# Optimization experiments

Measured on AMD Instinct MI355X. Metric: run time of the kernel, lower is better.

The kernel has to match this reference:

```python
import jax, jax.numpy as jnp
import numpy as np
import math

B, S, D = 4, 512, 2048
NH, DEG = 8, 4            # chebyshev heads / degree
HD = D // NH              # 256
AH = 16                   # attention heads
AHD = D // AH             # 128
W = 512                   # local attention window
BASE_LR = 0.005

def rmsnorm(x, w, eps=1e-6):
    return x * jax.lax.rsqrt(jnp.mean(x * x, axis=-1, keepdims=True) + eps) * w

def cheby_rkv(xn, coeffs, momentum, gate, ema):
    # Chebyshev spectral read + EMA/TTT coefficient update (apply_cheby_rkv_v10)
    Bb, Ss, Dd = xn.shape
    u = xn.reshape(Bb, Ss, NH, HD)
    z = jnp.tanh(u.mean(-1))                       # (B,S,NH) in [-1,1]
    Ts = [jnp.ones_like(z), z]
    for _ in range(DEG - 2):
        Ts.append(2.0 * z * Ts[-1] - Ts[-2])       # Chebyshev recurrence
    T = jnp.stack(Ts[:DEG], axis=-1)               # (B,S,NH,DEG)
    out = jnp.einsum('bshk,bhkd->bshd', T, coeffs).reshape(Bb, Ss, Dd)
    grad = jnp.einsum('bshk,bshd->bhkd', T, u) / Ss
    mom = ema * momentum + (1.0 - ema) * grad
    coeffs_new = coeffs + BASE_LR * gate[:, :, None, None] * mom
    return out, coeffs_new, mom

def local_attention(q, k, v):
    # q,k,v: (B,H,S,hd); causal attention within a sliding window of W
    Bb, H, Ss, hd = q.shape
    nc = Ss // W
    q = q.reshape(Bb, H, nc, W, hd)
    k = k.reshape(Bb, H, nc, W, hd)
    v = v.reshape(Bb, H, nc, W, hd)
    kprev = jnp.concatenate([jnp.zeros_like(k[:, :, :1]), k[:, :, :-1]], axis=2)
    vprev = jnp.concatenate([jnp.zeros_like(v[:, :, :1]), v[:, :, :-1]], axis=2)
    kk = jnp.concatenate([kprev, k], axis=3)       # (B,H,nc,2W,hd)
    vv = jnp.concatenate([vprev, v], axis=3)
    qi = jnp.arange(W)
    kj = jnp.arange(2 * W)
    causal = (kj[None, :] - W) <= qi[:, None]      # (W,2W)
    chunk_ok = (jnp.arange(nc)[:, None, None] > 0) | (kj[None, None, :] >= W)
    mask = causal[None] & chunk_ok                 # (nc,W,2W)
    scores = jnp.einsum('bhnqd,bhnkd->bhnqk', q, kk) / math.sqrt(hd)
    scores = jnp.where(mask[None, None], scores, -1e9)
    attn = jax.nn.softmax(scores, axis=-1)
    o = jnp.einsum('bhnqk,bhnkd->bhnqd', attn, vv)
    return o.reshape(Bb, H, Ss, hd)

def _forward(x, w_in, wg1, bg1, wg2, bg2, wc1, bc1, wc2, bc2,
             wq, wk, wv, wo, w_nc, w_ns, w_fgv, w_np, w_out):
    Bb, Ss, Dd = x.shape
    xn = rmsnorm(x, w_in)
    x_mean = xn.mean(axis=1)                       # (B,D)
    # coeff init (cheby_state is None): MLP + spectral 1/(k+1) scaling
    h = jax.nn.silu(x_mean @ wc1 + bc1)
    coeff_raw = h @ wc2 + bc2
    kidx = jnp.arange(DEG, dtype=jnp.float32)
    spectral_scale = (0.1 / (kidx + 1.0)).reshape(1, 1, DEG, 1)
    coeffs = coeff_raw.reshape(Bb, NH, DEG, HD) * spectral_scale
    momentum = jnp.zeros_like(coeffs)
    # complexity gate (GatedComplexityPredictor)
    g = jax.nn.silu(x_mean @ wg1 + bg1)
    gate_global = jax.nn.sigmoid(g @ wg2 + bg2)    # (B,1)
    # EMA momentum schedule: total_tokens_seen = S after this call
    progress = min(Ss / 1e8, 1.0)
    ema = 0.7 + 0.5 * (0.9 - 0.7) * (1.0 + math.cos(progress * math.pi))
    cheby_out, coeffs, momentum = cheby_rkv(xn, coeffs, momentum, gate_global, ema)
    # SLR: windowed local attention, keys/values conditioned on cheby output
    kv_src = xn + cheby_out
    q = (xn @ wq).reshape(Bb, Ss, AH, AHD).transpose(0, 2, 1, 3)
    k = (kv_src @ wk).reshape(Bb, Ss, AH, AHD).transpose(0, 2, 1, 3)
    v = (kv_src @ wv).reshape(Bb, Ss, AH, AHD).transpose(0, 2, 1, 3)
    slr = local_attention(q, k, v).transpose(0, 2, 1, 3).reshape(Bb, Ss, Dd) @ wo
    # gated SwiGLU-style fusion of the two paths
    h1 = rmsnorm(cheby_out, w_nc)
    h2 = rmsnorm(slr, w_ns)
    gv = jnp.concatenate([h1, h2], axis=-1) @ w_fgv
    gate, value = gv[..., :Dd], gv[..., Dd:]
    fused = rmsnorm(jax.nn.silu(gate) * value, w_np)
    return x + fused @ w_out

def setup_inputs() -> dict:
    key = jax.random.key(0)
    ks = jax.random.split(key, 12)
    s = 0.02
    return {
        'x': jax.random.normal(ks[0], (B, S, D), jnp.float32),
        'w_in': jnp.ones((D,), jnp.float32),
        'wg1': jax.random.normal(ks[1], (D, D // 4), jnp.float32) * s,
        'bg1': jnp.zeros((D // 4,), jnp.float32),
        'wg2': jax.random.normal(ks[2], (D // 4, 1), jnp.float32) * s,
        'bg2': jnp.zeros((1,), jnp.float32),
        'wc1': jax.random.normal(ks[3], (D, D // 4), jnp.float32) * s,
        'bc1': jnp.zeros((D // 4,), jnp.float32),
        'wc2': jax.random.normal(ks[4], (D // 4, NH * DEG * HD), jnp.float32) * s,
        'bc2': jnp.zeros((NH * DEG * HD,), jnp.float32),
        'wq': jax.random.normal(ks[5], (D, D), jnp.float32) * s,
        'wk': jax.random.normal(ks[6], (D, D), jnp.float32) * s,
        'wv': jax.random.normal(ks[7], (D, D), jnp.float32) * s,
        'wo': jax.random.normal(ks[8], (D, D), jnp.float32) * s,
        'w_nc': jnp.ones((D,), jnp.float32),
        'w_ns': jnp.ones((D,), jnp.float32),
        'w_fgv': jax.random.normal(ks[9], (2 * D, 2 * D), jnp.float32) * s,
        'w_np': jnp.ones((D,), jnp.float32),
        'w_out': jax.random.normal(ks[10], (D, D), jnp.float32) * s,
    }

def reference(x, w_in, wg1, bg1, wg2, bg2, wc1, bc1, wc2, bc2,
              wq, wk, wv, wo, w_nc, w_ns, w_fgv, w_np, w_out):
    return _forward(x, w_in, wg1, bg1, wg2, bg2, wc1, bc1, wc2, bc2,
                    wq, wk, wv, wo, w_nc, w_ns, w_fgv, w_np, w_out)
```

## Files before the change

kernel.cpp:

```cpp
#include <hip/hip_runtime.h>
#include <hip/hip_bf16.h>
#include <math.h>

#define Bz 4
#define Sz 512
#define Dz 2048
#define NHz 8
#define DEGz 4
#define HDz 256
#define AHz 16
#define AHDz 128
#define SCALE_ATT 0.08838834764831845f

typedef __attribute__((ext_vector_type(8))) short short8;
typedef __attribute__((ext_vector_type(4))) float f32x4;

#define AS1 __attribute__((address_space(1)))
#define AS3 __attribute__((address_space(3)))

__device__ inline void gload16(const void* g, void* l) {
    __builtin_amdgcn_global_load_lds((const AS1 void*)g, (AS3 void*)l, 16, 0, 0);
}

struct GOp {
    const void* A; const void* B; void* C; const float* add;
    long long sAb, sAh, sBb, sBh, sCb, sCh;
    int K, lda, ldb, ldc, nbh, gx, gy, flags, tileEnd;
};
struct GArgs { int n; GOp op[6]; };

__global__ __launch_bounds__(256) void gemm_multi(GArgs ga) {
    __shared__ unsigned short As[2 * 128 * 32];
    __shared__ unsigned short Bs[2 * 128 * 32];

    int tid = blockIdx.x;
    int oi = 0;
    while (tid >= ga.op[oi].tileEnd) ++oi;
    GOp o = ga.op[oi];
    int local = tid - (oi ? ga.op[oi - 1].tileEnd : 0);
    int t = threadIdx.x;

    if (o.flags & 32) {
        const float* src = (const float*)o.A;
        __hip_bfloat16* dst = (__hip_bfloat16*)o.C;
        int ty = local / o.gx, tx = local - ty * o.gx;
        int k0 = ty * 32, n0 = tx * 32;
        float* tile = (float*)As;
        int c = t & 31, r8 = t >> 5;
#pragma unroll
        for (int p = 0; p < 4; ++p)
            tile[(r8 + p * 8) * 33 + c] = src[(long long)(k0 + r8 + p * 8) * o.lda + n0 + c];
        __syncthreads();
#pragma unroll
        for (int p = 0; p < 4; ++p)
            dst[(long long)(n0 + r8 + p * 8) * o.ldc + k0 + c] =
                __float2bfloat16(tile[c * 33 + r8 + p * 8]);
        return;
    }

    int perOp = o.gx * o.gy;
    int batch = local / perOp;
    int r3 = local - batch * perOp;
    int ty = r3 / o.gx;
    int tx = r3 - ty * o.gx;
    int row0 = ty * 128, col0 = tx * 128;

    if ((o.flags & 4) && (col0 > row0 + 127)) return;

    int zb = batch / o.nbh, zh = batch - zb * o.nbh;
    long long cb = (long long)zb * o.sCb + (long long)zh * o.sCh;

    int kEnd = o.K;
    if (o.flags & 8) { int ke = row0 + 128; kEnd = kEnd < ke ? kEnd : ke; }

    const unsigned short* Ab = (const unsigned short*)o.A + zb * o.sAb + zh * o.sAh;
    const unsigned short* Bb = (const unsigned short*)o.B + zb * o.sBb + zh * o.sBh;

    int w = t >> 6, l = t & 63;
    int lrow = l >> 2;
    int lchunk = (l & 3) * 8;

    const unsigned short* aP0 = Ab + (long long)(row0 + w * 16 + lrow) * o.lda + lchunk;
    const unsigned short* aP1 = aP0 + 64LL * o.lda;
    const unsigned short* bP0 = Bb + (long long)(col0 + w * 16 + lrow) * o.ldb + lchunk;
    const unsigned short* bP1 = bP0 + 64LL * o.ldb;
    unsigned short* aL0 = As + w * 512;
    unsigned short* aL1 = As + (w + 4) * 512;
    unsigned short* bL0 = Bs + w * 512;
    unsigned short* bL1 = Bs + (w + 4) * 512;

    int lm = l & 15, lq = l >> 4;
    int wr = (w >> 1) * 64, wc = (w & 1) * 64;

    f32x4 acc[4][4];
#pragma unroll
    for (int i = 0; i < 4; ++i)
#pragma unroll
        for (int j = 0; j < 4; ++j) acc[i][j] = (f32x4){0.f, 0.f, 0.f, 0.f};

    for (int k0 = 0; k0 < kEnd; k0 += 64) {
        gload16(aP0, aL0);
        gload16(aP1, aL1);
        gload16(bP0, bL0);
        gload16(bP1, bL1);
        gload16(aP0 + 32, aL0 + 4096);
        gload16(aP1 + 32, aL1 + 4096);
        gload16(bP0 + 32, bL0 + 4096);
        gload16(bP1 + 32, bL1 + 4096);
        aP0 += 64; aP1 += 64; bP0 += 64; bP1 += 64;
        __syncthreads();

#pragma unroll
        for (int h = 0; h < 2; ++h) {
            const unsigned short* Ah = As + h * 4096;
            const unsigned short* Bh = Bs + h * 4096;
            short8 af[4], bfr[4];
#pragma unroll
            for (int i = 0; i < 4; ++i)
                af[i] = *(const short8*)(Ah + (wr + i * 16 + lm) * 32 + lq * 8);
#pragma unroll
            for (int j = 0; j < 4; ++j)
                bfr[j] = *(const short8*)(Bh + (wc + j * 16 + lm) * 32 + lq * 8);
#pragma unroll
            for (int i = 0; i < 4; ++i)
#pragma unroll
                for (int j = 0; j < 4; ++j)
                    acc[i][j] = __builtin_amdgcn_mfma_f32_16x16x32_bf16(af[i], bfr[j], acc[i][j], 0, 0, 0);
        }
        __syncthreads();
    }

    if (o.flags & 1) {
        __hip_bfloat16* C = (__hip_bfloat16*)o.C;
#pragma unroll
        for (int i = 0; i < 4; ++i)
#pragma unroll
            for (int j = 0; j < 4; ++j)
#pragma unroll
                for (int r = 0; r < 4; ++r) {
                    int grow = row0 + wr + i * 16 + lq * 4 + r;
                    int gcol = col0 + wc + j * 16 + lm;
                    float v = acc[i][j][r];
                    if (o.flags & 4) v = (gcol > grow) ? -1e9f : v * SCALE_ATT;
                    C[cb + (long long)grow * o.ldc + gcol] = __float2bfloat16(v);
                }
    } else {
        float* C = (float*)o.C;
#pragma unroll
        for (int i = 0; i < 4; ++i)
#pragma unroll
            for (int j = 0; j < 4; ++j)
#pragma unroll
                for (int r = 0; r < 4; ++r) {
                    int grow = row0 + wr + i * 16 + lq * 4 + r;
                    int gcol = col0 + wc + j * 16 + lm;
                    float v = acc[i][j][r];
                    long long ci = cb + (long long)grow * o.ldc + gcol;
                    if (o.flags & 2) v += o.add[ci];
                    C[ci] = v;
                }
    }
}

__global__ __launch_bounds__(512) void gemm_dp(GArgs ga) {
    __shared__ unsigned short As[2][128 * 64];
    __shared__ unsigned short Bs[2][256 * 64];

    int tid = blockIdx.x;
    int oi = 0;
    while (tid >= ga.op[oi].tileEnd) ++oi;
    GOp o = ga.op[oi];
    int local = tid - (oi ? ga.op[oi - 1].tileEnd : 0);
    int t = threadIdx.x;

    int perOp = o.gx * o.gy;
    int batch = local / perOp;
    int r3 = local - batch * perOp;
    int ty = r3 / o.gx, tx = r3 - ty * o.gx;
    int row0 = ty * 128, col0 = tx * 256;

    int zb = batch / o.nbh, zh = batch - zb * o.nbh;
    long long cb = (long long)zb * o.sCb + (long long)zh * o.sCh;

    const unsigned short* Ab = (const unsigned short*)o.A + zb * o.sAb + zh * o.sAh;
    const unsigned short* Bb = (const unsigned short*)o.B + zb * o.sBb + zh * o.sBh;

    int w = t >> 6, l = t & 63;
    int srow = w * 8 + (l >> 3);
    int scol = ((l & 7) ^ (l >> 3)) << 3;

    const unsigned short* aS0 = Ab + (long long)(row0 + srow) * o.lda + scol;
    const unsigned short* aS1 = Ab + (long long)(row0 + 64 + srow) * o.lda + scol;
    const unsigned short* bS0 = Bb + (long long)(col0 + srow) * o.ldb + scol;
    const unsigned short* bS1 = Bb + (long long)(col0 + 64 + srow) * o.ldb + scol;
    const unsigned short* bS2 = Bb + (long long)(col0 + 128 + srow) * o.ldb + scol;
    const unsigned short* bS3 = Bb + (long long)(col0 + 192 + srow) * o.ldb + scol;

    int wofs = w * 512;

    gload16(aS0, &As[0][wofs]);
    gload16(aS1, &As[0][4096 + wofs]);
    gload16(bS0, &Bs[0][wofs]);
    gload16(bS1, &Bs[0][4096 + wofs]);
    gload16(bS2, &Bs[0][8192 + wofs]);
    gload16(bS3, &Bs[0][12288 + wofs]);
    aS0 += 64; aS1 += 64; bS0 += 64; bS1 += 64; bS2 += 64; bS3 += 64;

    int lm = l & 15, lq = l >> 4;
    int wr = w >> 2, wc = w & 3;
    int c0 = ((lq) ^ (lm & 7)) << 3;
    int c1 = ((4 + lq) ^ (lm & 7)) << 3;

    f32x4 acc[4][4];
#pragma unroll
    for (int i = 0; i < 4; ++i)
#pragma unroll
        for (int j = 0; j < 4; ++j) acc[i][j] = (f32x4){0.f, 0.f, 0.f, 0.f};

    int nkt = o.K >> 6;
    for (int kt = 0; kt < nkt; ++kt) {
        unsigned short* Ac = &As[kt & 1][0];
        unsigned short* Bc = &Bs[kt & 1][0];
        unsigned short* An = &As[(kt & 1) ^ 1][0];
        unsigned short* Bn = &Bs[(kt & 1) ^ 1][0];

        if (kt + 1 < nkt) {
            gload16(aS0, An + wofs);
            gload16(aS1, An + 4096 + wofs);
            gload16(bS0, Bn + wofs);
            asm volatile("s_waitcnt vmcnt(3)" ::: "memory");
        } else {
            asm volatile("s_waitcnt vmcnt(0)" ::: "memory");
        }
        __builtin_amdgcn_s_barrier();
        __builtin_amdgcn_sched_barrier(0);

        short8 a0[2][2], b0[4][2];
#pragma unroll
        for (int mi = 0; mi < 2; ++mi) {
            const unsigned short* ar = Ac + (wr * 64 + mi * 16 + lm) * 64;
            a0[mi][0] = *(const short8*)(ar + c0);
            a0[mi][1] = *(const short8*)(ar + c1);
        }
#pragma unroll
        for (int nj = 0; nj < 4; ++nj) {
            const unsigned short* br = Bc + (wc * 64 + nj * 16 + lm) * 64;
            b0[nj][0] = *(const short8*)(br + c0);
            b0[nj][1] = *(const short8*)(br + c1);
        }
        __builtin_amdgcn_s_setprio(1);
#pragma unroll
        for (int kh = 0; kh < 2; ++kh)
#pragma unroll
            for (int mi = 0; mi < 2; ++mi)
#pragma unroll
                for (int nj = 0; nj < 4; ++nj)
                    acc[mi][nj] = __builtin_amdgcn_mfma_f32_16x16x32_bf16(a0[mi][kh], b0[nj][kh], acc[mi][nj], 0, 0, 0);
        __builtin_amdgcn_s_setprio(0);

        if (kt + 1 < nkt) {
            gload16(bS1, Bn + 4096 + wofs);
            gload16(bS2, Bn + 8192 + wofs);
            gload16(bS3, Bn + 12288 + wofs);
            aS0 += 64; aS1 += 64; bS0 += 64; bS1 += 64; bS2 += 64; bS3 += 64;
        }
        short8 a1[2][2];
#pragma unroll
        for (int mi = 0; mi < 2; ++mi) {
            const unsigned short* ar = Ac + (wr * 64 + (mi + 2) * 16 + lm) * 64;
            a1[mi][0] = *(const short8*)(ar + c0);
            a1[mi][1] = *(const short8*)(ar + c1);
        }
        __builtin_amdgcn_s_setprio(1);
#pragma unroll
        for (int kh = 0; kh < 2; ++kh)
#pragma unroll
            for (int mi = 0; mi < 2; ++mi)
#pragma unroll
                for (int nj = 0; nj < 4; ++nj)
                    acc[mi + 2][nj] = __builtin_amdgcn_mfma_f32_16x16x32_bf16(a1[mi][kh], b0[nj][kh], acc[mi + 2][nj], 0, 0, 0);
        __builtin_amdgcn_s_setprio(0);
        __builtin_amdgcn_sched_barrier(0);
        __builtin_amdgcn_s_barrier();
        __builtin_amdgcn_sched_barrier(0);
    }

    if (o.flags & 1) {
        __hip_bfloat16* C = (__hip_bfloat16*)o.C;
#pragma unroll
        for (int i = 0; i < 4; ++i)
#pragma unroll
            for (int j = 0; j < 4; ++j)
#pragma unroll
                for (int r = 0; r < 4; ++r) {
                    int grow = row0 + wr * 64 + i * 16 + lq * 4 + r;
                    int gcol = col0 + wc * 64 + j * 16 + lm;
                    C[cb + (long long)grow * o.ldc + gcol] = __float2bfloat16(acc[i][j][r]);
                }
    } else {
        float* C = (float*)o.C;
#pragma unroll
        for (int i = 0; i < 4; ++i)
#pragma unroll
            for (int j = 0; j < 4; ++j)
#pragma unroll
                for (int r = 0; r < 4; ++r) {
                    int grow = row0 + wr * 64 + i * 16 + lq * 4 + r;
                    int gcol = col0 + wc * 64 + j * 16 + lm;
                    float v = acc[i][j][r];
                    long long ci = cb + (long long)grow * o.ldc + gcol;
                    if (o.flags & 2) v += o.add[ci];
                    C[ci] = v;
                }
    }
}

__global__ __launch_bounds__(256) void rmsnorm_kernel(const float* __restrict__ x,
                                                      const float* __restrict__ w,
                                                      __hip_bfloat16* __restrict__ out) {
    long long base = (long long)blockIdx.x * Dz;
    int t = threadIdx.x;
    float v[8];
    float ss = 0.f;
#pragma unroll
    for (int p = 0; p < 8; ++p) { v[p] = x[base + t + p * 256]; ss += v[p] * v[p]; }
    __shared__ float red[256];
    red[t] = ss; __syncthreads();
    for (int s2 = 128; s2 > 0; s2 >>= 1) { if (t < s2) red[t] += red[t + s2]; __syncthreads(); }
    float sc = rsqrtf(red[0] / (float)Dz + 1e-6f);
#pragma unroll
    for (int p = 0; p < 8; ++p) { int c = t + p * 256; out[base + c] = __float2bfloat16(v[p] * sc * w[c]); }
}

__global__ __launch_bounds__(256) void xmean_p1(const __hip_bfloat16* __restrict__ xn,
                                                float* __restrict__ xmp) {
    int blk = blockIdx.x;
    int b = blk >> 6, sc = (blk >> 3) & 7, dc = blk & 7;
    int t = threadIdx.x;
    int d = dc * 256 + t;
    const __hip_bfloat16* p = xn + (long long)b * Sz * Dz + (long long)sc * 64 * Dz + d;
    float s = 0.f;
    for (int si = 0; si < 64; ++si) s += __bfloat162float(p[(long long)si * Dz]);
    xmp[(b * 8 + sc) * Dz + d] = s;
}

__global__ __launch_bounds__(256) void mlp1_kernel(const float* __restrict__ xmp,
                                                   const float* __restrict__ wc1,
                                                   const float* __restrict__ bc1,
                                                   float* __restrict__ h) {
    int blk = blockIdx.x;
    int b = blk >> 4, jb = blk & 15;
    int t = threadIdx.x;
    __shared__ float xs[Dz];
    __shared__ float red[8][32];
    const float* P = xmp + b * 8 * Dz;
#pragma unroll
    for (int p = 0; p < 8; ++p) {
        int d = t + p * 256;
        float s = 0.f;
#pragma unroll
        for (int q = 0; q < 8; ++q) s += P[q * Dz + d];
        xs[d] = s * (1.0f / (float)Sz);
    }
    __syncthreads();
    int j = jb * 32 + (t & 31), ksl = t >> 5;
    float s = 0.f;
    for (int k = ksl * 256; k < ksl * 256 + 256; ++k)
        s += xs[k] * wc1[(long long)k * 512 + j];
    red[ksl][t & 31] = s;
    __syncthreads();
    if (t < 32) {
        float tot = 0.f;
#pragma unroll
        for (int q = 0; q < 8; ++q) tot += red[q][t];
        tot += bc1[jb * 32 + t];
        h[b * 512 + jb * 32 + t] = tot / (1.0f + expf(-tot));
    }
}

__global__ __launch_bounds__(256) void coeffs_kernel(const float* __restrict__ h,
                                                     const float* __restrict__ wc2,
                                                     const float* __restrict__ bc2,
                                                     float* __restrict__ coeffs) {
    int blk = blockIdx.x;
    int b = blk >> 7, ib = blk & 127;
    int t = threadIdx.x;
    int i = ib * 64 + (t & 63), ksl = t >> 6;
    const float* hb = h + b * 512;
    float s = 0.f;
    for (int k = ksl * 128; k < ksl * 128 + 128; ++k)
        s += hb[k] * wc2[(long long)k * 8192 + i];
    __shared__ float red[4][64];
    red[ksl][t & 63] = s;
    __syncthreads();
    if (t < 64) {
        int ii = ib * 64 + t;
        float tot = red[0][t] + red[1][t] + red[2][t] + red[3][t] + bc2[ii];
        int kdeg = (ii >> 8) & 3;
        coeffs[b * 8192 + ii] = tot * (0.1f / (float)(kdeg + 1));
    }
}

__global__ __launch_bounds__(256) void cheby_kernel(const __hip_bfloat16* __restrict__ xn,
                                                    const float* __restrict__ coeffs,
                                                    __hip_bfloat16* __restrict__ cheby_out,
                                                    __hip_bfloat16* __restrict__ kv_src) {
    int bs = blockIdx.x;
    int b = bs >> 9;
    long long base = (long long)bs * Dz;
    int t = threadIdx.x;
    __shared__ float xrow[Dz];
    __shared__ float hsum[NHz][33];
    __shared__ float T[NHz][4];
#pragma unroll
    for (int p = 0; p < 8; ++p) xrow[t + p * 256] = __bfloat162float(xn[base + t + p * 256]);
    __syncthreads();
    int hh = t >> 5, lane = t & 31;
    float s = 0.f;
#pragma unroll
    for (int q = 0; q < 8; ++q) s += xrow[hh * HDz + lane + q * 32];
    hsum[hh][lane] = s;
    __syncthreads();
    if (t < NHz) {
        float tot = 0.f;
        for (int l2 = 0; l2 < 32; ++l2) tot += hsum[t][l2];
        float z = tanhf(tot / (float)HDz);
        float t2 = 2.f * z * z - 1.f;
        T[t][0] = 1.f; T[t][1] = z; T[t][2] = t2; T[t][3] = 2.f * z * t2 - z;
    }
    __syncthreads();
    const float* cbp = coeffs + (long long)b * (NHz * DEGz * HDz);
#pragma unroll
    for (int p = 0; p < 8; ++p) {
        int e = t + p * 256;
        int hd = e >> 8;
        int d = e & (HDz - 1);
        const float* ch = cbp + hd * (DEGz * HDz) + d;
        float co = T[hd][0] * ch[0] + T[hd][1] * ch[HDz] + T[hd][2] * ch[2 * HDz] + T[hd][3] * ch[3 * HDz];
        cheby_out[base + e] = __float2bfloat16(co);
        kv_src[base + e] = __float2bfloat16(xrow[e] + co);
    }
}

__global__ __launch_bounds__(128) void softmax_kernel(__hip_bfloat16* __restrict__ sc) {
    long long rid = blockIdx.x;
    int i = (int)(rid & (Sz - 1));
    long long base = rid * Sz;
    int t = threadIdx.x;
    float vals[4];
    float mx = -1e30f;
#pragma unroll
    for (int p = 0; p < 4; ++p) {
        int j = t + p * 128;
        float v = __bfloat162float(sc[base + j]);
        if (j > i) v = -1e9f;
        vals[p] = v;
        mx = fmaxf(mx, v);
    }
    __shared__ float red[128];
    red[t] = mx; __syncthreads();
    for (int s2 = 64; s2 > 0; s2 >>= 1) { if (t < s2) red[t] = fmaxf(red[t], red[t + s2]); __syncthreads(); }
    mx = red[0]; __syncthreads();
    float sum = 0.f;
#pragma unroll
    for (int p = 0; p < 4; ++p) { vals[p] = __expf(vals[p] - mx); sum += vals[p]; }
    red[t] = sum; __syncthreads();
    for (int s2 = 64; s2 > 0; s2 >>= 1) { if (t < s2) red[t] += red[t + s2]; __syncthreads(); }
    float inv = 1.0f / red[0];
#pragma unroll
    for (int p = 0; p < 4; ++p) sc[base + t + p * 128] = __float2bfloat16(vals[p] * inv);
}

__global__ __launch_bounds__(256) void hcat_kernel(const __hip_bfloat16* __restrict__ cheby,
                                                   const __hip_bfloat16* __restrict__ slr,
                                                   const float* __restrict__ w_nc,
                                                   const float* __restrict__ w_ns,
                                                   __hip_bfloat16* __restrict__ hcat) {
    long long row = blockIdx.x;
    const __hip_bfloat16* c = cheby + row * Dz;
    const __hip_bfloat16* sl = slr + row * Dz;
    __hip_bfloat16* o = hcat + row * (2 * Dz);
    int t = threadIdx.x;
    float v1[8], v2[8];
    float ss1 = 0.f, ss2 = 0.f;
#pragma unroll
    for (int p = 0; p < 8; ++p) {
        v1[p] = __bfloat162float(c[t + p * 256]);  ss1 += v1[p] * v1[p];
        v2[p] = __bfloat162float(sl[t + p * 256]); ss2 += v2[p] * v2[p];
    }
    __shared__ float red[256];
    red[t] = ss1; __syncthreads();
    for (int s2 = 128; s2 > 0; s2 >>= 1) { if (t < s2) red[t] += red[t + s2]; __syncthreads(); }
    float sc1 = rsqrtf(red[0] / (float)Dz + 1e-6f);
    __syncthreads();
    red[t] = ss2; __syncthreads();
    for (int s2 = 128; s2 > 0; s2 >>= 1) { if (t < s2) red[t] += red[t + s2]; __syncthreads(); }
    float sc2 = rsqrtf(red[0] / (float)Dz + 1e-6f);
#pragma unroll
    for (int p = 0; p < 8; ++p) {
        int cx = t + p * 256;
        o[cx] = __float2bfloat16(v1[p] * sc1 * w_nc[cx]);
        o[Dz + cx] = __float2bfloat16(v2[p] * sc2 * w_ns[cx]);
    }
}

__global__ __launch_bounds__(256) void fusedgate_kernel(const __hip_bfloat16* __restrict__ gv,
                                                        const float* __restrict__ w_np,
                                                        __hip_bfloat16* __restrict__ fused) {
    long long row = blockIdx.x;
    const __hip_bfloat16* g = gv + row * (2 * Dz);
    __hip_bfloat16* o = fused + row * Dz;
    int t = threadIdx.x;
    float f[8];
    float ss = 0.f;
#pragma unroll
    for (int p = 0; p < 8; ++p) {
        float ga = __bfloat162float(g[t + p * 256]);
        float va = __bfloat162float(g[Dz + t + p * 256]);
        float sv = ga / (1.0f + expf(-ga)) * va;
        f[p] = sv; ss += sv * sv;
    }
    __shared__ float red[256];
    red[t] = ss; __syncthreads();
    for (int s2 = 128; s2 > 0; s2 >>= 1) { if (t < s2) red[t] += red[t + s2]; __syncthreads(); }
    float sc = rsqrtf(red[0] / (float)Dz + 1e-6f);
#pragma unroll
    for (int p = 0; p < 8; ++p) { int cx = t + p * 256; o[cx] = __float2bfloat16(f[p] * sc * w_np[cx]); }
}

static GOp gop(const void* A, const void* B, void* C, const float* add,
               int K, int lda, int ldb, int ldc, int nbh, int nb, int gx, int gy,
               long long sAb, long long sAh, long long sBb, long long sBh,
               long long sCb, long long sCh, int flags) {
    GOp o;
    o.A = A; o.B = B; o.C = C; o.add = add;
    o.sAb = sAb; o.sAh = sAh; o.sBb = sBb; o.sBh = sBh; o.sCb = sCb; o.sCh = sCh;
    o.K = K; o.lda = lda; o.ldb = ldb; o.ldc = ldc; o.nbh = nbh;
    o.gx = gx; o.gy = gy; o.flags = flags;
    o.tileEnd = (flags & 32) ? gx * gy : nb * gx * gy;
    return o;
}

static void launch_multi(hipStream_t st, GOp* ops, int n) {
    GArgs ga; ga.n = n;
    int acc = 0;
    for (int i = 0; i < n; ++i) { acc += ops[i].tileEnd; ga.op[i] = ops[i]; ga.op[i].tileEnd = acc; }
    hipLaunchKernelGGL(gemm_multi, dim3(acc), dim3(256), 0, st, ga);
}

static void launch_dp(hipStream_t st, GOp* ops, int n) {
    GArgs ga; ga.n = n;
    int acc = 0;
    for (int i = 0; i < n; ++i) { acc += ops[i].tileEnd; ga.op[i] = ops[i]; ga.op[i].tileEnd = acc; }
    hipLaunchKernelGGL(gemm_dp, dim3(acc), dim3(512), 0, st, ga);
}

extern "C" void kernel_launch(void* const* d_in, const int* in_sizes, int n_in,
                              void* d_out, int out_size, void* d_ws, size_t ws_size,
                              hipStream_t stream) {
    const float* x     = (const float*)d_in[0];
    const float* w_in  = (const float*)d_in[1];
    const float* wc1   = (const float*)d_in[6];
    const float* bc1   = (const float*)d_in[7];
    const float* wc2   = (const float*)d_in[8];
    const float* bc2   = (const float*)d_in[9];
    const float* wq    = (const float*)d_in[10];
    const float* wk    = (const float*)d_in[11];
    const float* wv    = (const float*)d_in[12];
    const float* wo    = (const float*)d_in[13];
    const float* w_nc  = (const float*)d_in[14];
    const float* w_ns  = (const float*)d_in[15];
    const float* w_fgv = (const float*)d_in[16];
    const float* w_np  = (const float*)d_in[17];
    const float* w_out = (const float*)d_in[18];
    float* out = (float*)d_out;

    const size_t MB = 1ull << 20;
    char* W = (char*)d_ws;
    __hip_bfloat16* xn_bf    = (__hip_bfloat16*)(W + 0 * MB);
    __hip_bfloat16* kv_bf    = (__hip_bfloat16*)(W + 8 * MB);
    __hip_bfloat16* cheby_bf = (__hip_bfloat16*)(W + 16 * MB);
    __hip_bfloat16* q_bf     = (__hip_bfloat16*)(W + 24 * MB);
    __hip_bfloat16* k_bf     = (__hip_bfloat16*)(W + 32 * MB);
    __hip_bfloat16* vT_bf    = (__hip_bfloat16*)(W + 40 * MB);
    __hip_bfloat16* o_bf     = (__hip_bfloat16*)(W + 48 * MB);
    __hip_bfloat16* scores   = (__hip_bfloat16*)(W + 56 * MB);
    __hip_bfloat16* wq_t     = (__hip_bfloat16*)(W + 88 * MB);
    __hip_bfloat16* wk_t     = (__hip_bfloat16*)(W + 96 * MB);
    __hip_bfloat16* wv_t     = (__hip_bfloat16*)(W + 104 * MB);
    __hip_bfloat16* wo_t     = (__hip_bfloat16*)(W + 112 * MB);
    __hip_bfloat16* wout_t   = (__hip_bfloat16*)(W + 120 * MB);
    __hip_bfloat16* wfgv_t   = (__hip_bfloat16*)(W + 56 * MB);
    __hip_bfloat16* slr_bf   = (__hip_bfloat16*)(W + 0 * MB);
    __hip_bfloat16* hcat_bf  = (__hip_bfloat16*)(W + 24 * MB);
    __hip_bfloat16* gv_bf    = (__hip_bfloat16*)(W + 40 * MB);
    __hip_bfloat16* fused_bf = (__hip_bfloat16*)(W + 8 * MB);
    float* xmp   = (float*)(W + 128 * MB);
    float* hbuf  = xmp + 65536;
    float* cbuf  = hbuf + 2048;

    const int BS = Bz * Sz;
    const long long SD = (long long)Sz * Dz;
    const long long SS = (long long)Sz * Sz;

    {
        GOp ops[5];
        const float* srcs[5] = {wq, wk, wv, wo, w_out};
        __hip_bfloat16* dsts[5] = {wq_t, wk_t, wv_t, wo_t, wout_t};
        for (int i = 0; i < 5; ++i)
            ops[i] = gop(srcs[i], nullptr, dsts[i], nullptr, Dz, Dz, 0, Dz,
                         1, 1, 64, 64, 0, 0, 0, 0, 0, 0, 32);
        launch_multi(stream, ops, 5);
    }
    hipLaunchKernelGGL(rmsnorm_kernel, dim3(BS), dim3(256), 0, stream, x, w_in, xn_bf);
    hipLaunchKernelGGL(xmean_p1, dim3(256), dim3(256), 0, stream, xn_bf, xmp);
    hipLaunchKernelGGL(mlp1_kernel, dim3(64), dim3(256), 0, stream, xmp, wc1, bc1, hbuf);
    hipLaunchKernelGGL(coeffs_kernel, dim3(512), dim3(256), 0, stream, hbuf, wc2, bc2, cbuf);
    hipLaunchKernelGGL(cheby_kernel, dim3(BS), dim3(256), 0, stream, xn_bf, cbuf, cheby_bf, kv_bf);
    {
        GOp ops[3];
        ops[0] = gop(xn_bf, wq_t, q_bf, nullptr, Dz, Dz, Dz, Dz, 1, 1, 8, 16,
                     0, 0, 0, 0, 0, 0, 1);
        ops[1] = gop(kv_bf, wk_t, k_bf, nullptr, Dz, Dz, Dz, Dz, 1, 1, 8, 16,
                     0, 0, 0, 0, 0, 0, 1);
        ops[2] = gop(wv_t, kv_bf, vT_bf, nullptr, Dz, Dz, Dz, Sz, 1, Bz, 2, 16,
                     0, 0, SD, 0, (long long)Dz * Sz, 0, 1);
        launch_dp(stream, ops, 3);
    }
    {
        GOp op = gop(q_bf, k_bf, scores, nullptr, AHDz, Dz, Dz, Sz, AHz, Bz * AHz, 4, 4,
                     SD, AHDz, SD, AHDz, (long long)AHz * SS, SS, 1 | 4);
        launch_multi(stream, &op, 1);
    }
    hipLaunchKernelGGL(softmax_kernel, dim3(Bz * AHz * Sz), dim3(128), 0, stream, scores);
    {
        GOp op = gop(scores, vT_bf, o_bf, nullptr, Sz, Sz, Sz, Dz, AHz, Bz * AHz, 1, 4,
                     (long long)AHz * SS, SS, (long long)Dz * Sz, 128LL * Sz,
                     SD, 128, 1 | 8);
        launch_multi(stream, &op, 1);
    }
    {
        GOp op = gop(w_fgv, nullptr, wfgv_t, nullptr, 2 * Dz, 2 * Dz, 0, 2 * Dz,
                     1, 1, 128, 128, 0, 0, 0, 0, 0, 0, 32);
        launch_multi(stream, &op, 1);
    }
    {
        GOp op = gop(o_bf, wo_t, slr_bf, nullptr, Dz, Dz, Dz, Dz, 1, 1, 8, 16,
                     0, 0, 0, 0, 0, 0, 1);
        launch_dp(stream, &op, 1);
    }
    hipLaunchKernelGGL(hcat_kernel, dim3(BS), dim3(256), 0, stream, cheby_bf, slr_bf, w_nc, w_ns, hcat_bf);
    {
        GOp op = gop(hcat_bf, wfgv_t, gv_bf, nullptr, 2 * Dz, 2 * Dz, 2 * Dz, 2 * Dz,
                     1, 1, 16, 16, 0, 0, 0, 0, 0, 0, 1);
        launch_dp(stream, &op, 1);
    }
    hipLaunchKernelGGL(fusedgate_kernel, dim3(BS), dim3(256), 0, stream, gv_bf, w_np, fused_bf);
    {
        GOp op = gop(fused_bf, wout_t, out, x, Dz, Dz, Dz, Dz, 1, 1, 8, 16,
                     0, 0, 0, 0, 0, 0, 2);
        launch_dp(stream, &op, 1);
    }
}
```

Baseline: 616.9 us.

## Triple-buffer gemm_dp LDS pipeline and merge wo GEMM with w_fgv transpose launch

Moves the dual-path GEMM kernel from double to triple buffering of its LDS tiles. Two k-tiles are now prefetched ahead, with vmcnt waits adjusted to match, so more memory latency can be hidden. Separately, the wo projection GEMM now runs inside the same multi-op launch as the w_fgv transpose, using the launch_multi path with a 16x16 grid instead of launch_dp. Shared memory per block grows to about 144KB, which can lower occupancy. The wo GEMM also switches kernels and tile mapping.

```diff
diff --git a/kernel.cpp b/kernel.cpp
--- a/kernel.cpp
+++ b/kernel.cpp
@@ -163,8 +163,8 @@
 }
 
 __global__ __launch_bounds__(512) void gemm_dp(GArgs ga) {
-    __shared__ unsigned short As[2][128 * 64];
-    __shared__ unsigned short Bs[2][256 * 64];
+    __shared__ unsigned short As[3][128 * 64];
+    __shared__ unsigned short Bs[3][256 * 64];
 
     int tid = blockIdx.x;
     int oi = 0;
@@ -197,6 +197,8 @@
     const unsigned short* bS3 = Bb + (long long)(col0 + 192 + srow) * o.ldb + scol;
 
     int wofs = w * 512;
+
+    int nkt = o.K >> 6;
 
     gload16(aS0, &As[0][wofs]);
     gload16(aS1, &As[0][4096 + wofs]);
@@ -205,6 +207,15 @@
     gload16(bS2, &Bs[0][8192 + wofs]);
     gload16(bS3, &Bs[0][12288 + wofs]);
     aS0 += 64; aS1 += 64; bS0 += 64; bS1 += 64; bS2 += 64; bS3 += 64;
+    if (nkt > 1) {
+        gload16(aS0, &As[1][wofs]);
+        gload16(aS1, &As[1][4096 + wofs]);
+        gload16(bS0, &Bs[1][wofs]);
+        gload16(bS1, &Bs[1][4096 + wofs]);
+        gload16(bS2, &Bs[1][8192 + wofs]);
+        gload16(bS3, &Bs[1][12288 + wofs]);
+        aS0 += 64; aS1 += 64; bS0 += 64; bS1 += 64; bS2 += 64; bS3 += 64;
+    }
 
     int lm = l & 15, lq = l >> 4;
     int wr = w >> 2, wc = w & 3;
@@ -217,21 +228,23 @@
 #pragma unroll
         for (int j = 0; j < 4; ++j) acc[i][j] = (f32x4){0.f, 0.f, 0.f, 0.f};
 
-    int nkt = o.K >> 6;
+    int cur = 0;
     for (int kt = 0; kt < nkt; ++kt) {
-        unsigned short* Ac = &As[kt & 1][0];
-        unsigned short* Bc = &Bs[kt & 1][0];
-        unsigned short* An = &As[(kt & 1) ^ 1][0];
-        unsigned short* Bn = &Bs[(kt & 1) ^ 1][0];
-
-        if (kt + 1 < nkt) {
+        int stg = cur + 2; if (stg >= 3) stg -= 3;
+        unsigned short* Ac = &As[cur][0];
+        unsigned short* Bc = &Bs[cur][0];
+        unsigned short* An = &As[stg][0];
+        unsigned short* Bn = &Bs[stg][0];
+
+        if (kt + 2 < nkt) {
             gload16(aS0, An + wofs);
             gload16(aS1, An + 4096 + wofs);
             gload16(bS0, Bn + wofs);
-            asm volatile("s_waitcnt vmcnt(3)" ::: "memory");
-        } else {
-            asm volatile("s_waitcnt vmcnt(0)" ::: "memory");
         }
+        __builtin_amdgcn_sched_barrier(0);
+        if (kt + 2 < nkt)      asm volatile("s_waitcnt vmcnt(9)" ::: "memory");
+        else if (kt + 1 < nkt) asm volatile("s_waitcnt vmcnt(6)" ::: "memory");
+        else                   asm volatile("s_waitcnt vmcnt(0)" ::: "memory");
         __builtin_amdgcn_s_barrier();
         __builtin_amdgcn_sched_barrier(0);
 
@@ -258,7 +271,7 @@
                     acc[mi][nj] = __builtin_amdgcn_mfma_f32_16x16x32_bf16(a0[mi][kh], b0[nj][kh], acc[mi][nj], 0, 0, 0);
         __builtin_amdgcn_s_setprio(0);
 
-        if (kt + 1 < nkt) {
+        if (kt + 2 < nkt) {
             gload16(bS1, Bn + 4096 + wofs);
             gload16(bS2, Bn + 8192 + wofs);
             gload16(bS3, Bn + 12288 + wofs);
@@ -283,6 +296,8 @@
         __builtin_amdgcn_sched_barrier(0);
         __builtin_amdgcn_s_barrier();
         __builtin_amdgcn_sched_barrier(0);
+
+        cur = cur + 1; if (cur >= 3) cur -= 3;
     }
 
     if (o.flags & 1) {
@@ -640,14 +655,12 @@
         launch_multi(stream, &op, 1);
     }
     {
-        GOp op = gop(w_fgv, nullptr, wfgv_t, nullptr, 2 * Dz, 2 * Dz, 0, 2 * Dz,
+        GOp ops[2];
+        ops[0] = gop(o_bf, wo_t, slr_bf, nullptr, Dz, Dz, Dz, Dz, 1, 1, 16, 16,
+                     0, 0, 0, 0, 0, 0, 1);
+        ops[1] = gop(w_fgv, nullptr, wfgv_t, nullptr, 2 * Dz, 2 * Dz, 0, 2 * Dz,
                      1, 1, 128, 128, 0, 0, 0, 0, 0, 0, 32);
-        launch_multi(stream, &op, 1);
-    }
-    {
-        GOp op = gop(o_bf, wo_t, slr_bf, nullptr, Dz, Dz, Dz, Dz, 1, 1, 8, 16,
-                     0, 0, 0, 0, 0, 0, 1);
-        launch_dp(stream, &op, 1);
+        launch_multi(stream, ops, 2);
     }
     hipLaunchKernelGGL(hcat_kernel, dim3(BS), dim3(256), 0, stream, cheby_bf, slr_bf, w_nc, w_ns, hcat_bf);
     {
```

Result: slower. 636.8 us (+3.2%).

## Split GEMM K-step into four quadrant MFMA phases and co-launch wo GEMM with transpose

Applied to the files above, without the earlier changes.

The GEMM inner loop is restructured into four MFMA quadrant phases. Each phase loads only the A/B fragments it needs from LDS, interleaves the next tile's global-to-LDS loads between phases, and adds workgroup barriers and explicit lgkmcnt waits to keep the waves in step. Separately, the wo projection GEMM is merged into the same multi-op launch as the w_fgv transpose, and it and the output GEMM switch from the data-parallel launcher to the multi launcher with a different tile/split setting. The intent is better overlap of LDS reads, global loads and MFMA work, plus fewer launches. In exchange it adds many more barriers per K step, which could stall waves.

```diff
diff --git a/kernel.cpp b/kernel.cpp
--- a/kernel.cpp
+++ b/kernel.cpp
@@ -223,62 +223,101 @@
         unsigned short* Bc = &Bs[kt & 1][0];
         unsigned short* An = &As[(kt & 1) ^ 1][0];
         unsigned short* Bn = &Bs[(kt & 1) ^ 1][0];
-
-        if (kt + 1 < nkt) {
+        bool pf = (kt + 1 < nkt);
+
+        if (pf) {
             gload16(aS0, An + wofs);
             gload16(aS1, An + 4096 + wofs);
-            gload16(bS0, Bn + wofs);
-            asm volatile("s_waitcnt vmcnt(3)" ::: "memory");
-        } else {
-            asm volatile("s_waitcnt vmcnt(0)" ::: "memory");
         }
+        __builtin_amdgcn_sched_barrier(0);
+        if (pf) asm volatile("s_waitcnt vmcnt(2)" ::: "memory");
+        else    asm volatile("s_waitcnt vmcnt(0)" ::: "memory");
         __builtin_amdgcn_s_barrier();
         __builtin_amdgcn_sched_barrier(0);
 
-        short8 a0[2][2], b0[4][2];
+        short8 aR0[2][2], aR1[2][2], bR0[2][2], bR1[2][2];
+
 #pragma unroll
         for (int mi = 0; mi < 2; ++mi) {
             const unsigned short* ar = Ac + (wr * 64 + mi * 16 + lm) * 64;
-            a0[mi][0] = *(const short8*)(ar + c0);
-            a0[mi][1] = *(const short8*)(ar + c1);
+            aR0[mi][0] = *(const short8*)(ar + c0);
+            aR0[mi][1] = *(const short8*)(ar + c1);
         }
 #pragma unroll
-        for (int nj = 0; nj < 4; ++nj) {
+        for (int nj = 0; nj < 2; ++nj) {
             const unsigned short* br = Bc + (wc * 64 + nj * 16 + lm) * 64;
-            b0[nj][0] = *(const short8*)(br + c0);
-            b0[nj][1] = *(const short8*)(br + c1);
+            bR0[nj][0] = *(const short8*)(br + c0);
+            bR0[nj][1] = *(const short8*)(br + c1);
         }
+        if (pf) gload16(bS0, Bn + wofs);
+        __builtin_amdgcn_s_barrier();
+        asm volatile("s_waitcnt lgkmcnt(0)" ::: "memory");
+        __builtin_amdgcn_sched_barrier(0);
         __builtin_amdgcn_s_setprio(1);
 #pragma unroll
         for (int kh = 0; kh < 2; ++kh)
 #pragma unroll
             for (int mi = 0; mi < 2; ++mi)
 #pragma unroll
-                for (int nj = 0; nj < 4; ++nj)
-                    acc[mi][nj] = __builtin_amdgcn_mfma_f32_16x16x32_bf16(a0[mi][kh], b0[nj][kh], acc[mi][nj], 0, 0, 0);
+                for (int nj = 0; nj < 2; ++nj)
+                    acc[mi][nj] = __builtin_amdgcn_mfma_f32_16x16x32_bf16(aR0[mi][kh], bR0[nj][kh], acc[mi][nj], 0, 0, 0);
         __builtin_amdgcn_s_setprio(0);
-
-        if (kt + 1 < nkt) {
-            gload16(bS1, Bn + 4096 + wofs);
+        __builtin_amdgcn_s_barrier();
+
+#pragma unroll
+        for (int nj = 0; nj < 2; ++nj) {
+            const unsigned short* br = Bc + (wc * 64 + (nj + 2) * 16 + lm) * 64;
+            bR1[nj][0] = *(const short8*)(br + c0);
+            bR1[nj][1] = *(const short8*)(br + c1);
+        }
+        if (pf) gload16(bS1, Bn + 4096 + wofs);
+        __builtin_amdgcn_s_barrier();
+        asm volatile("s_waitcnt lgkmcnt(0)" ::: "memory");
+        __builtin_amdgcn_sched_barrier(0);
+        __builtin_amdgcn_s_setprio(1);
+#pragma unroll
+        for (int kh = 0; kh < 2; ++kh)
+#pragma unroll
+            for (int mi = 0; mi < 2; ++mi)
+#pragma unroll
+                for (int nj = 0; nj < 2; ++nj)
+                    acc[mi][nj + 2] = __builtin_amdgcn_mfma_f32_16x16x32_bf16(aR0[mi][kh], bR1[nj][kh], acc[mi][nj + 2], 0, 0, 0);
+        __builtin_amdgcn_s_setprio(0);
+        __builtin_amdgcn_s_barrier();
+
+#pragma unroll
+        for (int mi = 0; mi < 2; ++mi) {
+            const unsigned short* ar = Ac + (wr * 64 + (mi + 2) * 16 + lm) * 64;
+            aR1[mi][0] = *(const short8*)(ar + c0);
+            aR1[mi][1] = *(const short8*)(ar + c1);
+        }
+        if (pf) {
             gload16(bS2, Bn + 8192 + wofs);
             gload16(bS3, Bn + 12288 + wofs);
             aS0 += 64; aS1 += 64; bS0 += 64; bS1 += 64; bS2 += 64; bS3 += 64;
         }
-        short8 a1[2][2];
-#pragma unroll
-        for (int mi = 0; mi < 2; ++mi) {
-            const unsigned short* ar = Ac + (wr * 64 + (mi + 2) * 16 + lm) * 64;
-            a1[mi][0] = *(const short8*)(ar + c0);
-            a1[mi][1] = *(const short8*)(ar + c1);
-        }
+        __builtin_amdgcn_s_barrier();
+        asm volatile("s_waitcnt lgkmcnt(0)" ::: "memory");
+        __builtin_amdgcn_sched_barrier(0);
         __builtin_amdgcn_s_setprio(1);
 #pragma unroll
         for (int kh = 0; kh < 2; ++kh)
 #pragma unroll
             for (int mi = 0; mi < 2; ++mi)
 #pragma unroll
-                for (int nj = 0; nj < 4; ++nj)
-                    acc[mi + 2][nj] = __builtin_amdgcn_mfma_f32_16x16x32_bf16(a1[mi][kh], b0[nj][kh], acc[mi + 2][nj], 0, 0, 0);
+                for (int nj = 0; nj < 2; ++nj)
+                    acc[mi + 2][nj] = __builtin_amdgcn_mfma_f32_16x16x32_bf16(aR1[mi][kh], bR0[nj][kh], acc[mi + 2][nj], 0, 0, 0);
+        __builtin_amdgcn_s_setprio(0);
+        __builtin_amdgcn_s_barrier();
+
+        __builtin_amdgcn_s_setprio(1);
+#pragma unroll
+        for (int kh = 0; kh < 2; ++kh)
+#pragma unroll
+            for (int mi = 0; mi < 2; ++mi)
+#pragma unroll
+                for (int nj = 0; nj < 2; ++nj)
+                    acc[mi + 2][nj + 2] = __builtin_amdgcn_mfma_f32_16x16x32_bf16(aR1[mi][kh], bR1[nj][kh], acc[mi + 2][nj + 2], 0, 0, 0);
         __builtin_amdgcn_s_setprio(0);
         __builtin_amdgcn_sched_barrier(0);
         __builtin_amdgcn_s_barrier();
@@ -640,14 +679,12 @@
         launch_multi(stream, &op, 1);
     }
     {
-        GOp op = gop(w_fgv, nullptr, wfgv_t, nullptr, 2 * Dz, 2 * Dz, 0, 2 * Dz,
+        GOp ops[2];
+        ops[0] = gop(o_bf, wo_t, slr_bf, nullptr, Dz, Dz, Dz, Dz, 1, 1, 16, 16,
+                     0, 0, 0, 0, 0, 0, 1);
+        ops[1] = gop(w_fgv, nullptr, wfgv_t, nullptr, 2 * Dz, 2 * Dz, 0, 2 * Dz,
                      1, 1, 128, 128, 0, 0, 0, 0, 0, 0, 32);
-        launch_multi(stream, &op, 1);
-    }
-    {
-        GOp op = gop(o_bf, wo_t, slr_bf, nullptr, Dz, Dz, Dz, Dz, 1, 1, 8, 16,
-                     0, 0, 0, 0, 0, 0, 1);
-        launch_dp(stream, &op, 1);
+        launch_multi(stream, ops, 2);
     }
     hipLaunchKernelGGL(hcat_kernel, dim3(BS), dim3(256), 0, stream, cheby_bf, slr_bf, w_nc, w_ns, hcat_bf);
     {
@@ -657,8 +694,8 @@
     }
     hipLaunchKernelGGL(fusedgate_kernel, dim3(BS), dim3(256), 0, stream, gv_bf, w_np, fused_bf);
     {
-        GOp op = gop(fused_bf, wout_t, out, x, Dz, Dz, Dz, Dz, 1, 1, 8, 16,
+        GOp op = gop(fused_bf, wout_t, out, x, Dz, Dz, Dz, Dz, 1, 1, 16, 16,
                      0, 0, 0, 0, 0, 0, 2);
-        launch_dp(stream, &op, 1);
-    }
-}
+        launch_multi(stream, &op, 1);
+    }
+}
```

After: 637.8 us. +3.4%, slower.
